# Kernel tuning notes

Hardware: AMD Instinct MI355X
Metric: run time of the kernel (lower is better)

## Reference

```python
import jax, jax.numpy as jnp
import numpy as np

B, M, D = 256, 196, 512


def setup_inputs() -> dict:
    key = jax.random.key(0)
    x = jax.random.normal(key, (B, M, D), dtype=jnp.float32)
    # learned temperature, initialized as in __init__: log(1/(2*M))
    t = jnp.log(jnp.full((1,), 1.0 / (2 * M), dtype=jnp.float32))
    return {"x": x, "t": t}


def reference(x, t):
    # x: [B, M, D] -> transpose to [B, D, M] as in BDCovpool
    xt = jnp.transpose(x, (0, 2, 1))
    dim = xt.shape[1]
    # gram[b,i,j] = <xt[b,i,:], xt[b,j,:]>  (x_pow2 in the original)
    gram = jnp.einsum('bim,bjm->bij', xt, xt)
    diag = jnp.diagonal(gram, axis1=1, axis2=2)  # [B, D]
    # I_M @ (g*I) + (g*I) @ I_M - 2g  ==  diag[j] + diag[i] - 2*gram  (banding)
    dcov = diag[:, None, :] + diag[:, :, None] - 2.0 * gram
    dcov = jnp.maximum(dcov, 0.0)
    dcov = jnp.sqrt(jnp.exp(t)[0] * dcov + 1e-5)
    # double centering: matmuls with all-ones I_M are row/col/total means * dim
    row = jnp.mean(dcov, axis=2, keepdims=True)
    col = jnp.mean(dcov, axis=1, keepdims=True)
    tot = jnp.mean(dcov, axis=(1, 2), keepdims=True)
    cent = dcov - row - col + tot  # [B, D, D]
    # Triuvec: row-major upper triangle (incl. diagonal) gather
    iu = jnp.triu_indices(dim)
    return cent[:, iu[0], iu[1]]  # [B, D*(D+1)/2]
```

## Files before the change

kernel.cpp:

```cpp
#include <hip/hip_runtime.h>
#include <hip/hip_bf16.h>
#include <math.h>

#define Bn 256
#define Mn 196
#define Dn 512
#define Mstr 232
#define TILE 128
#define OUTB 131328

typedef __attribute__((ext_vector_type(8))) short bf16x8;
typedef __attribute__((ext_vector_type(4))) float f32x4;

__device__ __forceinline__ unsigned short f2bf(float f) {
  unsigned u = __float_as_uint(f);
  unsigned r = u + 0x7fffu + ((u >> 16) & 1u);
  return (unsigned short)(r >> 16);
}

__device__ __forceinline__ void stage_panel(short* __restrict__ lds,
                                            float* __restrict__ dtmp,
                                            const float* __restrict__ xb,
                                            int c0, int tid) {
  const int c = tid & 127;
  float dacc = 0.f;
  #pragma unroll
  for (int it = 0; it < 4; ++it) {
    const int mc = (tid >> 7) + 8 * it;
    if (mc < 28) {
      const int m0 = mc * 8;
      float xv[8];
      #pragma unroll
      for (int u = 0; u < 8; ++u) {
        const int m = m0 + u;
        xv[u] = (m < Mn) ? xb[(size_t)m * Dn + c0 + c] : 0.f;
        dacc += xv[u] * xv[u];
      }
      uint4 pk;
      pk.x = ((unsigned)f2bf(xv[1]) << 16) | (unsigned)f2bf(xv[0]);
      pk.y = ((unsigned)f2bf(xv[3]) << 16) | (unsigned)f2bf(xv[2]);
      pk.z = ((unsigned)f2bf(xv[5]) << 16) | (unsigned)f2bf(xv[4]);
      pk.w = ((unsigned)f2bf(xv[7]) << 16) | (unsigned)f2bf(xv[6]);
      *reinterpret_cast<uint4*>(&lds[c * Mstr + m0]) = pk;
    }
  }
  dtmp[tid] = dacc;
}

__global__ __launch_bounds__(1024)
void k1_gram_dcov(const float* __restrict__ x, const float* __restrict__ tptr,
                  float* __restrict__ out, float* __restrict__ rowsum) {
  __shared__ short ldsI[TILE * Mstr];
  __shared__ short ldsJ[TILE * Mstr];
  __shared__ float dtmp[1024];
  __shared__ float dI[TILE];
  __shared__ float dJ[TILE];

  const int tid = threadIdx.x;
  const int bid = blockIdx.x;
  const int ti  = bid >> 8;
  const int b   = bid & 255;
  const float* xb = x + (size_t)b * Mn * Dn;
  const float et = expf(tptr[0]);

  stage_panel(ldsI, dtmp, xb, ti * TILE, tid);
  __syncthreads();
  if (tid < TILE) {
    float s = 0.f;
    #pragma unroll
    for (int p = 0; p < 8; ++p) s += dtmp[p * 128 + tid];
    dI[tid] = s;
  }
  __syncthreads();

  const int lane = tid & 63;
  const int wid  = tid >> 6;
  const int wi = wid >> 2, wj = wid & 3;
  const int lr = lane & 15, lg = lane >> 4;
  const size_t outb = (size_t)b * OUTB;

  for (int tj = ti; tj < 4; ++tj) {
    const short* Bp;
    const float* dJv;
    if (tj > ti) {
      stage_panel(ldsJ, dtmp, xb, tj * TILE, tid);
      __syncthreads();
      if (tid < TILE) {
        float s = 0.f;
        #pragma unroll
        for (int p = 0; p < 8; ++p) s += dtmp[p * 128 + tid];
        dJ[tid] = s;
      }
      __syncthreads();
      Bp = ldsJ; dJv = dJ;
    } else {
      Bp = ldsI; dJv = dI;
    }

    f32x4 acc[2][2];
    #pragma unroll
    for (int a = 0; a < 2; ++a)
      #pragma unroll
      for (int c = 0; c < 2; ++c) acc[a][c] = (f32x4){0.f, 0.f, 0.f, 0.f};

    #pragma unroll
    for (int kk = 0; kk < 7; ++kk) {
      const int k0 = kk * 32 + lg * 8;
      bf16x8 af[2], bfr[2];
      #pragma unroll
      for (int mi = 0; mi < 2; ++mi)
        af[mi] = *reinterpret_cast<const bf16x8*>(&ldsI[(wi * 32 + mi * 16 + lr) * Mstr + k0]);
      #pragma unroll
      for (int nj = 0; nj < 2; ++nj)
        bfr[nj] = *reinterpret_cast<const bf16x8*>(&Bp[(wj * 32 + nj * 16 + lr) * Mstr + k0]);
      #pragma unroll
      for (int mi = 0; mi < 2; ++mi)
        #pragma unroll
        for (int nj = 0; nj < 2; ++nj)
          acc[mi][nj] = __builtin_amdgcn_mfma_f32_16x16x32_bf16(af[mi], bfr[nj], acc[mi][nj], 0, 0, 0);
    }

    float colAcc[2] = {0.f, 0.f};
    #pragma unroll
    for (int mi = 0; mi < 2; ++mi) {
      #pragma unroll
      for (int reg = 0; reg < 4; ++reg) {
        const int iloc = wi * 32 + mi * 16 + lg * 4 + reg;
        const int ig = ti * TILE + iloc;
        float rowAcc = 0.f;
        #pragma unroll
        for (int nj = 0; nj < 2; ++nj) {
          const int jloc = wj * 32 + nj * 16 + lr;
          const int jg = tj * TILE + jloc;
          float g = acc[mi][nj][reg];
          float raw = dI[iloc] + dJv[jloc] - 2.f * g;
          raw = fmaxf(raw, 0.f);
          if (ig == jg) raw = 0.f;
          const float v = sqrtf(et * raw + 1e-5f);
          if (ig <= jg) {
            const int off = ig * Dn - (ig * (ig - 1)) / 2;
            out[outb + off + (jg - ig)] = v;
            rowAcc += v;
            if (ig < jg) colAcc[nj] += v;
          }
        }
        rowAcc += __shfl_xor(rowAcc, 1);
        rowAcc += __shfl_xor(rowAcc, 2);
        rowAcc += __shfl_xor(rowAcc, 4);
        rowAcc += __shfl_xor(rowAcc, 8);
        if (lr == 0) atomicAdd(&rowsum[b * Dn + ig], rowAcc);
      }
    }
    #pragma unroll
    for (int nj = 0; nj < 2; ++nj) {
      float cs = colAcc[nj];
      cs += __shfl_xor(cs, 16);
      cs += __shfl_xor(cs, 32);
      if (lg == 0) {
        const int jg = tj * TILE + wj * 32 + nj * 16 + lr;
        atomicAdd(&rowsum[b * Dn + jg], cs);
      }
    }
    __syncthreads();
  }
}

__global__ __launch_bounds__(256)
void k2a_tot(const float* __restrict__ rowsum, float* __restrict__ tot) {
  const int b = blockIdx.x;
  const int t = threadIdx.x;
  float v = rowsum[b * Dn + t] + rowsum[b * Dn + t + 256];
  #pragma unroll
  for (int m = 1; m < 64; m <<= 1) v += __shfl_xor(v, m);
  __shared__ float w[4];
  if ((t & 63) == 0) w[t >> 6] = v;
  __syncthreads();
  if (t == 0) tot[b] = w[0] + w[1] + w[2] + w[3];
}

__global__ __launch_bounds__(256)
void k2_center(float* __restrict__ out, const float* __restrict__ rowsum,
               const float* __restrict__ tot) {
  const float inv = 1.f / 512.f;
  const int t = threadIdx.x;
  for (int r = blockIdx.x; r < Bn * Dn; r += gridDim.x) {
    const int b = r >> 9, i = r & 511;
    const float c0 = tot[b] * (1.f / (512.f * 512.f)) - rowsum[b * Dn + i] * inv;
    const int L = Dn - i;
    const size_t base = (size_t)b * OUTB + (size_t)(i * Dn - (i * (i - 1)) / 2);
    float* p = out + base;
    const float* rs = rowsum + b * Dn + i;
    int head = (int)((4 - (base & 3)) & 3);
    if (head > L) head = L;
    if (t < head) p[t] += c0 - rs[t] * inv;
    const int nb = (L - head) >> 2;
    for (int q = t; q < nb; q += 256) {
      const int s = head + q * 4;
      float4 v = *reinterpret_cast<float4*>(p + s);
      v.x += c0 - rs[s]     * inv;
      v.y += c0 - rs[s + 1] * inv;
      v.z += c0 - rs[s + 2] * inv;
      v.w += c0 - rs[s + 3] * inv;
      *reinterpret_cast<float4*>(p + s) = v;
    }
    const int s2 = head + nb * 4 + t;
    if (s2 < L) p[s2] += c0 - rs[s2] * inv;
  }
}

extern "C" void kernel_launch(void* const* d_in, const int* in_sizes, int n_in,
                              void* d_out, int out_size, void* d_ws, size_t ws_size,
                              hipStream_t stream) {
  const float* x = (const float*)d_in[0];
  const float* t = (const float*)d_in[1];
  float* out = (float*)d_out;
  float* rowsum = (float*)d_ws;
  float* tot = rowsum + Bn * Dn;

  hipMemsetAsync(rowsum, 0, Bn * Dn * sizeof(float), stream);
  hipLaunchKernelGGL(k1_gram_dcov, dim3(1024), dim3(1024), 0, stream, x, t, out, rowsum);
  hipLaunchKernelGGL(k2a_tot, dim3(Bn), dim3(256), 0, stream, rowsum, tot);
  hipLaunchKernelGGL(k2_center, dim3(4096), dim3(256), 0, stream, out, rowsum, tot);
}
```

Baseline: 350.1 us.

## Fuse gram, dcov, and centering into one per-batch kernel with recompute

Replaces the three-kernel pipeline (gram+dcov write, total reduction, centering read-modify-write) with one block per batch. The block computes the tile pairs twice: a first pass accumulates row sums in LDS, and a second pass recomputes the gram tiles and writes the centered output directly. Panel loads from global are software-pipelined into registers ahead of the MFMA work. This removes the output round trip, the global atomics and the memset, but doubles the MFMA and panel-load work and drops the grid from 1024 blocks to 256, which may reduce occupancy.

```diff
diff --git a/kernel.cpp b/kernel.cpp
--- a/kernel.cpp
+++ b/kernel.cpp
@@ -12,112 +12,110 @@
 typedef __attribute__((ext_vector_type(8))) short bf16x8;
 typedef __attribute__((ext_vector_type(4))) float f32x4;
 
-__device__ __forceinline__ unsigned short f2bf(float f) {
-  unsigned u = __float_as_uint(f);
-  unsigned r = u + 0x7fffu + ((u >> 16) & 1u);
-  return (unsigned short)(r >> 16);
+__device__ __forceinline__ unsigned pack2(float a, float b) {
+  __hip_bfloat16 ha = __float2bfloat16(a);
+  __hip_bfloat16 hb = __float2bfloat16(b);
+  unsigned short lo = *reinterpret_cast<unsigned short*>(&ha);
+  unsigned short hi = *reinterpret_cast<unsigned short*>(&hb);
+  return ((unsigned)hi << 16) | (unsigned)lo;
 }
 
-__device__ __forceinline__ void stage_panel(short* __restrict__ lds,
-                                            float* __restrict__ dtmp,
-                                            const float* __restrict__ xb,
-                                            int c0, int tid) {
-  const int c = tid & 127;
-  float dacc = 0.f;
-  #pragma unroll
-  for (int it = 0; it < 4; ++it) {
-    const int mc = (tid >> 7) + 8 * it;
-    if (mc < 28) {
-      const int m0 = mc * 8;
-      float xv[8];
-      #pragma unroll
-      for (int u = 0; u < 8; ++u) {
-        const int m = m0 + u;
-        xv[u] = (m < Mn) ? xb[(size_t)m * Dn + c0 + c] : 0.f;
-        dacc += xv[u] * xv[u];
-      }
-      uint4 pk;
-      pk.x = ((unsigned)f2bf(xv[1]) << 16) | (unsigned)f2bf(xv[0]);
-      pk.y = ((unsigned)f2bf(xv[3]) << 16) | (unsigned)f2bf(xv[2]);
-      pk.z = ((unsigned)f2bf(xv[5]) << 16) | (unsigned)f2bf(xv[4]);
-      pk.w = ((unsigned)f2bf(xv[7]) << 16) | (unsigned)f2bf(xv[6]);
-      *reinterpret_cast<uint4*>(&lds[c * Mstr + m0]) = pk;
-    }
-  }
-  dtmp[tid] = dacc;
-}
-
 __global__ __launch_bounds__(1024)
-void k1_gram_dcov(const float* __restrict__ x, const float* __restrict__ tptr,
-                  float* __restrict__ out, float* __restrict__ rowsum) {
-  __shared__ short ldsI[TILE * Mstr];
-  __shared__ short ldsJ[TILE * Mstr];
+void k1_fused(const float* __restrict__ x, const float* __restrict__ tptr,
+              float* __restrict__ out) {
+  __shared__ short bufA[TILE * Mstr];
+  __shared__ short bufB[TILE * Mstr];
   __shared__ float dtmp[1024];
-  __shared__ float dI[TILE];
-  __shared__ float dJ[TILE];
+  __shared__ float dAll[512];
+  __shared__ float rowsumL[512];
+  __shared__ float totL;
 
   const int tid = threadIdx.x;
-  const int bid = blockIdx.x;
-  const int ti  = bid >> 8;
-  const int b   = bid & 255;
+  const int b = blockIdx.x;
   const float* xb = x + (size_t)b * Mn * Dn;
   const float et = expf(tptr[0]);
-
-  stage_panel(ldsI, dtmp, xb, ti * TILE, tid);
-  __syncthreads();
-  if (tid < TILE) {
-    float s = 0.f;
-    #pragma unroll
-    for (int p = 0; p < 8; ++p) s += dtmp[p * 128 + tid];
-    dI[tid] = s;
-  }
-  __syncthreads();
+  const size_t outb = (size_t)b * OUTB;
 
   const int lane = tid & 63;
   const int wid  = tid >> 6;
   const int wi = wid >> 2, wj = wid & 3;
   const int lr = lane & 15, lg = lane >> 4;
-  const size_t outb = (size_t)b * OUTB;
-
-  for (int tj = ti; tj < 4; ++tj) {
-    const short* Bp;
-    const float* dJv;
-    if (tj > ti) {
-      stage_panel(ldsJ, dtmp, xb, tj * TILE, tid);
-      __syncthreads();
-      if (tid < TILE) {
+  const int c = tid & 127;
+  const int w = tid >> 7;
+
+  if (tid < 512) rowsumL[tid] = 0.f;
+
+  float xv[4][8];
+
+  auto pload = [&](int c0) {
+    #pragma unroll
+    for (int it = 0; it < 4; ++it) {
+      const int mc = w + 8 * it;
+      #pragma unroll
+      for (int u = 0; u < 8; ++u) {
+        const int m = mc * 8 + u;
+        xv[it][u] = (mc < 28 && m < Mn) ? xb[(size_t)m * Dn + c0 + c] : 0.f;
+      }
+    }
+  };
+
+  auto pstore = [&](short* buf, int pan, bool dg) {
+    __syncthreads();
+    float dacc = 0.f;
+    #pragma unroll
+    for (int it = 0; it < 4; ++it) {
+      const int mc = w + 8 * it;
+      if (mc < 28) {
+        if (dg) {
+          #pragma unroll
+          for (int u = 0; u < 8; ++u) dacc += xv[it][u] * xv[it][u];
+        }
+        uint4 pk;
+        pk.x = pack2(xv[it][0], xv[it][1]);
+        pk.y = pack2(xv[it][2], xv[it][3]);
+        pk.z = pack2(xv[it][4], xv[it][5]);
+        pk.w = pack2(xv[it][6], xv[it][7]);
+        *reinterpret_cast<uint4*>(&buf[c * Mstr + mc * 8]) = pk;
+      }
+    }
+    if (dg) dtmp[tid] = dacc;
+    __syncthreads();
+    if (dg) {
+      if (tid < 128) {
         float s = 0.f;
         #pragma unroll
         for (int p = 0; p < 8; ++p) s += dtmp[p * 128 + tid];
-        dJ[tid] = s;
+        dAll[pan * 128 + tid] = s;
       }
       __syncthreads();
-      Bp = ldsJ; dJv = dJ;
-    } else {
-      Bp = ldsI; dJv = dI;
-    }
-
+    }
+  };
+
+  auto cpair = [&](int ti, int tj, const short* bI, const short* bJ,
+                   bool passB, float ctot) {
+    const float* dI = dAll + ti * TILE;
+    const float* dJ = dAll + tj * TILE;
     f32x4 acc[2][2];
     #pragma unroll
     for (int a = 0; a < 2; ++a)
       #pragma unroll
-      for (int c = 0; c < 2; ++c) acc[a][c] = (f32x4){0.f, 0.f, 0.f, 0.f};
+      for (int cc = 0; cc < 2; ++cc) acc[a][cc] = (f32x4){0.f, 0.f, 0.f, 0.f};
 
     #pragma unroll
     for (int kk = 0; kk < 7; ++kk) {
       const int k0 = kk * 32 + lg * 8;
-      bf16x8 af[2], bfr[2];
+      bf16x8 af[2], bfv[2];
       #pragma unroll
       for (int mi = 0; mi < 2; ++mi)
-        af[mi] = *reinterpret_cast<const bf16x8*>(&ldsI[(wi * 32 + mi * 16 + lr) * Mstr + k0]);
+        af[mi] = *reinterpret_cast<const bf16x8*>(&bI[(wi * 32 + mi * 16 + lr) * Mstr + k0]);
       #pragma unroll
       for (int nj = 0; nj < 2; ++nj)
-        bfr[nj] = *reinterpret_cast<const bf16x8*>(&Bp[(wj * 32 + nj * 16 + lr) * Mstr + k0]);
+        bfv[nj] = *reinterpret_cast<const bf16x8*>(&bJ[(wj * 32 + nj * 16 + lr) * Mstr + k0]);
       #pragma unroll
       for (int mi = 0; mi < 2; ++mi)
         #pragma unroll
         for (int nj = 0; nj < 2; ++nj)
-          acc[mi][nj] = __builtin_amdgcn_mfma_f32_16x16x32_bf16(af[mi], bfr[nj], acc[mi][nj], 0, 0, 0);
+          acc[mi][nj] = __builtin_amdgcn_mfma_f32_16x16x32_bf16(af[mi], bfv[nj], acc[mi][nj], 0, 0, 0);
     }
 
     float colAcc[2] = {0.f, 0.f};
@@ -133,79 +131,90 @@
           const int jloc = wj * 32 + nj * 16 + lr;
           const int jg = tj * TILE + jloc;
           float g = acc[mi][nj][reg];
-          float raw = dI[iloc] + dJv[jloc] - 2.f * g;
+          float raw = dI[iloc] + dJ[jloc] - 2.f * g;
           raw = fmaxf(raw, 0.f);
           if (ig == jg) raw = 0.f;
           const float v = sqrtf(et * raw + 1e-5f);
-          if (ig <= jg) {
-            const int off = ig * Dn - (ig * (ig - 1)) / 2;
-            out[outb + off + (jg - ig)] = v;
-            rowAcc += v;
-            if (ig < jg) colAcc[nj] += v;
+          if (!passB) {
+            if (ig <= jg) rowAcc += v;
+            if (ig <  jg) colAcc[nj] += v;
+          } else if (ig <= jg) {
+            const float wv = v - (rowsumL[ig] + rowsumL[jg]) * (1.f / 512.f) + ctot;
+            out[outb + ig * Dn - (ig * (ig - 1)) / 2 + (jg - ig)] = wv;
           }
         }
-        rowAcc += __shfl_xor(rowAcc, 1);
-        rowAcc += __shfl_xor(rowAcc, 2);
-        rowAcc += __shfl_xor(rowAcc, 4);
-        rowAcc += __shfl_xor(rowAcc, 8);
-        if (lr == 0) atomicAdd(&rowsum[b * Dn + ig], rowAcc);
-      }
-    }
-    #pragma unroll
-    for (int nj = 0; nj < 2; ++nj) {
-      float cs = colAcc[nj];
-      cs += __shfl_xor(cs, 16);
-      cs += __shfl_xor(cs, 32);
-      if (lg == 0) {
-        const int jg = tj * TILE + wj * 32 + nj * 16 + lr;
-        atomicAdd(&rowsum[b * Dn + jg], cs);
-      }
-    }
-    __syncthreads();
+        if (!passB) {
+          rowAcc += __shfl_xor(rowAcc, 1);
+          rowAcc += __shfl_xor(rowAcc, 2);
+          rowAcc += __shfl_xor(rowAcc, 4);
+          rowAcc += __shfl_xor(rowAcc, 8);
+          if (lr == 0) atomicAdd(&rowsumL[ig], rowAcc);
+        }
+      }
+    }
+    if (!passB) {
+      #pragma unroll
+      for (int nj = 0; nj < 2; ++nj) {
+        float cs = colAcc[nj];
+        cs += __shfl_xor(cs, 16);
+        cs += __shfl_xor(cs, 32);
+        if (lg == 0) atomicAdd(&rowsumL[tj * TILE + wj * 32 + nj * 16 + lr], cs);
+      }
+    }
+  };
+
+  pload(0);                       pstore(bufA, 0, true);
+  pload(128);                     pstore(bufB, 1, true);
+  pload(256);
+  cpair(0,0,bufA,bufA,false,0.f); cpair(0,1,bufA,bufB,false,0.f); cpair(1,1,bufB,bufB,false,0.f);
+  pstore(bufB, 2, true);
+  pload(384);
+  cpair(0,2,bufA,bufB,false,0.f); cpair(2,2,bufB,bufB,false,0.f);
+  pstore(bufB, 3, true);
+  pload(128);
+  cpair(0,3,bufA,bufB,false,0.f); cpair(3,3,bufB,bufB,false,0.f);
+  pstore(bufA, 1, false);
+  pload(256);
+  cpair(1,3,bufA,bufB,false,0.f);
+  pstore(bufB, 2, false);
+  pload(384);
+  cpair(1,2,bufA,bufB,false,0.f);
+  pstore(bufA, 3, false);
+  cpair(2,3,bufB,bufA,false,0.f);
+
+  __syncthreads();
+  if (tid < 512) {
+    float v = rowsumL[tid];
+    #pragma unroll
+    for (int m = 1; m < 64; m <<= 1) v += __shfl_xor(v, m);
+    if ((tid & 63) == 0) dtmp[tid >> 6] = v;
   }
-}
-
-__global__ __launch_bounds__(256)
-void k2a_tot(const float* __restrict__ rowsum, float* __restrict__ tot) {
-  const int b = blockIdx.x;
-  const int t = threadIdx.x;
-  float v = rowsum[b * Dn + t] + rowsum[b * Dn + t + 256];
-  #pragma unroll
-  for (int m = 1; m < 64; m <<= 1) v += __shfl_xor(v, m);
-  __shared__ float w[4];
-  if ((t & 63) == 0) w[t >> 6] = v;
   __syncthreads();
-  if (t == 0) tot[b] = w[0] + w[1] + w[2] + w[3];
-}
-
-__global__ __launch_bounds__(256)
-void k2_center(float* __restrict__ out, const float* __restrict__ rowsum,
-               const float* __restrict__ tot) {
-  const float inv = 1.f / 512.f;
-  const int t = threadIdx.x;
-  for (int r = blockIdx.x; r < Bn * Dn; r += gridDim.x) {
-    const int b = r >> 9, i = r & 511;
-    const float c0 = tot[b] * (1.f / (512.f * 512.f)) - rowsum[b * Dn + i] * inv;
-    const int L = Dn - i;
-    const size_t base = (size_t)b * OUTB + (size_t)(i * Dn - (i * (i - 1)) / 2);
-    float* p = out + base;
-    const float* rs = rowsum + b * Dn + i;
-    int head = (int)((4 - (base & 3)) & 3);
-    if (head > L) head = L;
-    if (t < head) p[t] += c0 - rs[t] * inv;
-    const int nb = (L - head) >> 2;
-    for (int q = t; q < nb; q += 256) {
-      const int s = head + q * 4;
-      float4 v = *reinterpret_cast<float4*>(p + s);
-      v.x += c0 - rs[s]     * inv;
-      v.y += c0 - rs[s + 1] * inv;
-      v.z += c0 - rs[s + 2] * inv;
-      v.w += c0 - rs[s + 3] * inv;
-      *reinterpret_cast<float4*>(p + s) = v;
-    }
-    const int s2 = head + nb * 4 + t;
-    if (s2 < L) p[s2] += c0 - rs[s2] * inv;
+  if (tid == 0) {
+    float s = 0.f;
+    #pragma unroll
+    for (int i = 0; i < 8; ++i) s += dtmp[i];
+    totL = s;
   }
+  __syncthreads();
+  const float ctot = totL * (1.f / (512.f * 512.f));
+
+  pload(128);
+  cpair(2,3,bufB,bufA,true,ctot);
+  pstore(bufA, 1, false);
+  pload(384);
+  cpair(1,2,bufA,bufB,true,ctot);
+  pstore(bufB, 3, false);
+  pload(0);
+  cpair(1,3,bufA,bufB,true,ctot);
+  pstore(bufA, 0, false);
+  pload(256);
+  cpair(0,3,bufA,bufB,true,ctot); cpair(3,3,bufB,bufB,true,ctot);
+  pstore(bufB, 2, false);
+  pload(128);
+  cpair(0,2,bufA,bufB,true,ctot); cpair(2,2,bufB,bufB,true,ctot);
+  pstore(bufB, 1, false);
+  cpair(0,0,bufA,bufA,true,ctot); cpair(0,1,bufA,bufB,true,ctot); cpair(1,1,bufB,bufB,true,ctot);
 }
 
 extern "C" void kernel_launch(void* const* d_in, const int* in_sizes, int n_in,
@@ -214,11 +223,5 @@
   const float* x = (const float*)d_in[0];
   const float* t = (const float*)d_in[1];
   float* out = (float*)d_out;
-  float* rowsum = (float*)d_ws;
-  float* tot = rowsum + Bn * Dn;
-
-  hipMemsetAsync(rowsum, 0, Bn * Dn * sizeof(float), stream);
-  hipLaunchKernelGGL(k1_gram_dcov, dim3(1024), dim3(1024), 0, stream, x, t, out, rowsum);
-  hipLaunchKernelGGL(k2a_tot, dim3(Bn), dim3(256), 0, stream, rowsum, tot);
-  hipLaunchKernelGGL(k2_center, dim3(4096), dim3(256), 0, stream, out, rowsum, tot);
+  hipLaunchKernelGGL(k1_fused, dim3(Bn), dim3(1024), 0, stream, x, t, out);
 }
```

Result: slower. 512.8 us (+46.5%).
